# Performance work log

Measured on AMD Instinct MI355X. Metric: run time of the kernel, lower is better.

The kernel has to match this reference:

```python
import jax, jax.numpy as jnp
import numpy as np

# Fixed production-scale dims (equal-size graphs -> no ragged padding needed)
B, NPG, C, H, L, FFN, NC = 16, 512, 128, 8, 4, 512, 4
D = C // H          # head dim = 16
T = NPG + 1         # +1 virtual graph token
EPG = 8192          # edges per graph (avg degree 16)
E = B * EPG


def _ln(x, g, b, eps=1e-5):
    m = x.mean(-1, keepdims=True)
    v = ((x - m) ** 2).mean(-1, keepdims=True)
    return (x - m) * jax.lax.rsqrt(v + eps) * g + b


def setup_inputs() -> dict:
    key = jax.random.key(0)
    ks = jax.random.split(key, 24)
    N = B * NPG
    node_feats = jax.random.normal(ks[0], (N, 3), jnp.float32)
    # intra-graph edges: local endpoints + per-graph node offset (matches batch_ptr math)
    local = jax.random.randint(ks[1], (2, B, EPG), 0, NPG)
    offs = (jnp.arange(B) * NPG)[None, :, None]
    edge_index = (local + offs).reshape(2, E)
    edge_attr = jax.random.randint(ks[2], (E,), 0, 10)

    def nrm(k, shape, scale=0.02):
        return jax.random.normal(k, shape, jnp.float32) * scale

    params = {
        "W_node": nrm(ks[3], (3, C), 0.3), "b_node": jnp.zeros((C,), jnp.float32),
        "graph_token": nrm(ks[4], (C,), 1.0),
        "edge_bias_table": nrm(ks[5], (11, H), 0.1).at[0].set(0.0),  # padding_idx=0
        "in_deg_emb": nrm(ks[6], (512, C)).at[0].set(0.0),           # padding_idx=0
        "out_deg_emb": nrm(ks[7], (512, C)).at[0].set(0.0),
        "vnode_bias": nrm(ks[8], (H,), 1.0),
        "Wq": nrm(ks[9], (L, C, C)), "bq": jnp.zeros((L, C), jnp.float32),
        "Wk": nrm(ks[10], (L, C, C)), "bk": jnp.zeros((L, C), jnp.float32),
        "Wv": nrm(ks[11], (L, C, C)), "bv": jnp.zeros((L, C), jnp.float32),
        "Wo": nrm(ks[12], (L, C, C)), "bo": jnp.zeros((L, C), jnp.float32),
        "ln1_g": jnp.ones((L, C), jnp.float32), "ln1_b": jnp.zeros((L, C), jnp.float32),
        "ln2_g": jnp.ones((L, C), jnp.float32), "ln2_b": jnp.zeros((L, C), jnp.float32),
        "W1": nrm(ks[13], (L, C, FFN)), "b1": jnp.zeros((L, FFN), jnp.float32),
        "W2": nrm(ks[14], (L, FFN, C)), "b2": jnp.zeros((L, C), jnp.float32),
        "normf_g": jnp.ones((C,), jnp.float32), "normf_b": jnp.zeros((C,), jnp.float32),
        "Wc1": nrm(ks[15], (C, C // 2)), "bc1": jnp.zeros((C // 2,), jnp.float32),
        "Wc2": nrm(ks[16], (C // 2, NC)), "bc2": jnp.zeros((NC,), jnp.float32),
    }
    return {"node_feats": node_feats, "edge_index": edge_index,
            "edge_attr": edge_attr, "num_graphs": B, **params}


def reference(node_feats, W_node, b_node, graph_token, edge_bias_table,
              in_deg_emb, out_deg_emb, vnode_bias,
              Wq, bq, Wk, bk, Wv, bv, Wo, bo,
              ln1_g, ln1_b, ln2_g, ln2_b, W1, b1, W2, b2,
              normf_g, normf_b, Wc1, bc1, Wc2, bc2,
              edge_index, edge_attr, num_graphs):
    N = node_feats.shape[0]
    npg = N // num_graphs
    t = npg + 1
    src, dst = edge_index[0], edge_index[1]
    # degree encoders (scatter_add of ones == segment_sum)
    in_deg = jnp.clip(jax.ops.segment_sum(jnp.ones_like(dst), dst, num_segments=N), 0, 511)
    out_deg = jnp.clip(jax.ops.segment_sum(jnp.ones_like(src), src, num_segments=N), 0, 511)
    x_enc = node_feats @ W_node + b_node + in_deg_emb[in_deg] + out_deg_emb[out_deg]
    # equal-size graphs with sorted batch ids -> padding loop is a reshape, mask all-False
    x = jnp.concatenate(
        [jnp.broadcast_to(graph_token, (num_graphs, 1, C)),
         x_enc.reshape(num_graphs, npg, C)], axis=1)  # [B, T, C]
    # attention bias: vnode row/col + scattered edge-attr embeddings
    bias = jnp.zeros((num_graphs, H, t, t), jnp.float32)
    bias = bias.at[:, :, 0, :].set(vnode_bias[None, :, None])
    bias = bias.at[:, :, :, 0].set(vnode_bias[None, :, None])
    eb = edge_bias_table[jnp.clip(edge_attr, 0, 9) + 1]  # [E, H]
    g = src // npg
    sl = src - g * npg + 1
    dl = dst - g * npg + 1
    bias = bias.at[g, :, sl, dl].add(eb)  # duplicate edges accumulate (scatter_add)
    scale = 1.0 / np.sqrt(D).astype(np.float32)
    for l in range(L):  # key_padding_mask is all-False here -> masked_fill is a no-op
        h = _ln(x, ln1_g[l], ln1_b[l])
        q = (h @ Wq[l] + bq[l]).reshape(num_graphs, t, H, D)
        k = (h @ Wk[l] + bk[l]).reshape(num_graphs, t, H, D)
        v = (h @ Wv[l] + bv[l]).reshape(num_graphs, t, H, D)
        scores = jnp.einsum('bthd,bshd->bhts', q, k) * scale + bias
        attn = jax.nn.softmax(scores, axis=-1)
        o = jnp.einsum('bhts,bshd->bthd', attn, v).reshape(num_graphs, t, C)
        x = x + o @ Wo[l] + bo[l]
        h2 = _ln(x, ln2_g[l], ln2_b[l])
        x = x + jax.nn.gelu(h2 @ W1[l] + b1[l], approximate=False) @ W2[l] + b2[l]
    x = _ln(x, normf_g, normf_b)
    gr = x[:, 0, :]  # virtual-node readout
    return jax.nn.gelu(gr @ Wc1 + bc1, approximate=False) @ Wc2 + bc2
```

## Files before the change

### kernel.cpp

```cpp
#include <hip/hip_runtime.h>
#include <hip/hip_bf16.h>

#define BB 16
#define NPG 512
#define CC 128
#define HH 8
#define LL 4
#define FFN 512
#define NCLS 4
#define DD 16
#define TT 513
#define EE 131072
#define NNODES 8192
#define ROWS (BB * TT)
#define ECAP 64
#define SP 544
#define BSTR 292

static constexpr size_t XROWS = (size_t)BB * TT;
static constexpr size_t XSZ   = XROWS * CC;
static constexpr size_t VTSZ  = (size_t)BB * HH * DD * SP;

typedef unsigned short ushort_t;
typedef __attribute__((ext_vector_type(8))) short short8;
typedef __attribute__((ext_vector_type(4))) float floatx4;

__device__ __forceinline__ float gelu_exact(float v) {
    return 0.5f * v * (1.0f + erff(v * 0.70710678118654752440f));
}
__device__ __forceinline__ ushort_t f2bf(float f) {
    union { float f; unsigned u; } c; c.f = f;
    unsigned u = c.u;
    return (ushort_t)((u + 0x7FFFu + ((u >> 16) & 1u)) >> 16);
}
__device__ __forceinline__ int swz(int row, int col, int stride) {
    int kb = col >> 3;
    return row * stride + (((kb ^ (row & 7)) << 3) | (col & 7));
}

__device__ __forceinline__ void qkv_stage4(const ushort_t* hs,
                                           const ushort_t* Wtq, const float* bq_,
                                           const ushort_t* Wtk, const float* bk_,
                                           const ushort_t* Wtv, const float* bv_,
                                           ushort_t* qb, ushort_t* kb, ushort_t* vt,
                                           int m0, int wave, int lq, int quad) {
    const short* hsS = (const short*)hs;
    int n0 = wave * 32;
    int c0 = n0 + lq, c1 = n0 + 16 + lq;
    const short* Ws[3] = {(const short*)Wtq, (const short*)Wtk, (const short*)Wtv};
    const float* bs[3] = {bq_, bk_, bv_};
    size_t rB0 = (size_t)(n0 + lq) * CC, rB1 = (size_t)(n0 + 16 + lq) * CC;

    #pragma unroll
    for (int m = 0; m < 3; ++m) {
        const short* W = Ws[m];
        floatx4 a0 = {0.f,0.f,0.f,0.f}, a1 = a0;
        #pragma unroll
        for (int k0 = 0; k0 < CC; k0 += 32) {
            short8 af = *(const short8*)(hsS + swz(lq, k0 + quad * 8, 128));
            short8 b0 = *(const short8*)(W + rB0 + k0 + quad * 8);
            short8 b1 = *(const short8*)(W + rB1 + k0 + quad * 8);
            a0 = __builtin_amdgcn_mfma_f32_16x16x32_bf16(af, b0, a0, 0, 0, 0);
            a1 = __builtin_amdgcn_mfma_f32_16x16x32_bf16(af, b1, a1, 0, 0, 0);
        }
        float bv0 = bs[m][c0], bv1 = bs[m][c1];
        #pragma unroll
        for (int rg = 0; rg < 4; ++rg) {
            int r = m0 + quad * 4 + rg;
            float v0 = a0[rg] + bv0;
            float v1 = a1[rg] + bv1;
            if (m == 0) {
                qb[(size_t)r * CC + c0] = f2bf(v0 * 0.25f);
                qb[(size_t)r * CC + c1] = f2bf(v1 * 0.25f);
            } else if (m == 1) {
                kb[(size_t)r * CC + c0] = f2bf(v0);
                kb[(size_t)r * CC + c1] = f2bf(v1);
            } else {
                int bg = r / TT;
                int s = r - bg * TT;
                vt[((size_t)(bg * HH + (c0 >> 4)) * DD + (c0 & 15)) * SP + s] = f2bf(v0);
                vt[((size_t)(bg * HH + (c1 >> 4)) * DD + (c1 & 15)) * SP + s] = f2bf(v1);
            }
        }
    }
}

__global__ __launch_bounds__(256) void deg_csr_tr_kernel(const int* __restrict__ ei,
                                                         const int* __restrict__ ea,
                                                         int* __restrict__ deg_in,
                                                         int* __restrict__ deg_out,
                                                         int* __restrict__ cnt,
                                                         int* __restrict__ ebuf,
                                                         const float* __restrict__ Wq,
                                                         const float* __restrict__ Wk,
                                                         const float* __restrict__ Wv,
                                                         const float* __restrict__ Wo,
                                                         const float* __restrict__ W1,
                                                         const float* __restrict__ W2,
                                                         ushort_t* __restrict__ wtqkvo,
                                                         ushort_t* __restrict__ wt1,
                                                         ushort_t* __restrict__ wt2) {
    int bid = blockIdx.x;
    int tid = threadIdx.x;
    if (bid < 512) {
        int e = bid * 256 + tid;
        int src = ei[e], dst = ei[EE + e];
        atomicAdd(&deg_out[src], 1);
        atomicAdd(&deg_in[dst], 1);
        int g = src >> 9;
        int sl = src - (g << 9) + 1;
        int dl = dst - (g << 9) + 1;
        int a = ea[e];
        a = (a < 0) ? 0 : (a > 9 ? 9 : a);
        a += 1;
        int row = g * TT + sl;
        int pos = atomicAdd(&cnt[row], 1);
        if (pos < ECAP) ebuf[(size_t)row * ECAP + pos] = dl | (a << 16);
        return;
    }
    int z = bid - 512;
    const float* src; ushort_t* dst; int K, N, tile;
    if (z < 64) {
        int zz = z >> 2; tile = z & 3;
        int k = zz >> 2, l = zz & 3;
        const float* s4[4] = {Wq, Wk, Wv, Wo};
        src = s4[k] + (size_t)l * CC * CC;
        dst = wtqkvo + (size_t)(k * 4 + l) * 16384;
        K = CC; N = CC;
    } else if (z < 128) {
        int l = (z - 64) >> 4; tile = (z - 64) & 15;
        src = W1 + (size_t)l * CC * FFN;
        dst = wt1 + (size_t)l * 65536;
        K = CC; N = FFN;
    } else {
        int l = (z - 128) >> 4; tile = (z - 128) & 15;
        src = W2 + (size_t)l * FFN * CC;
        dst = wt2 + (size_t)l * 65536;
        K = FFN; N = CC;
    }
    int tilesN = N >> 6;
    int k0 = (tile / tilesN) << 6;
    int n0 = (tile - (tile / tilesN) * tilesN) << 6;
    __shared__ float t[64][65];
    int c = tid & 63, rb = tid >> 6;
    #pragma unroll
    for (int kk = 0; kk < 64; kk += 4)
        t[kk + rb][c] = src[(size_t)(k0 + kk + rb) * N + n0 + c];
    __syncthreads();
    #pragma unroll
    for (int nn = 0; nn < 64; nn += 4)
        dst[(size_t)(n0 + nn + rb) * K + k0 + c] = f2bf(t[c][nn + rb]);
}

__global__ __launch_bounds__(256) void encode_pre_kernel(const float* __restrict__ nf,
                                                         const float* __restrict__ Wn,
                                                         const float* __restrict__ bn,
                                                         const float* __restrict__ gt,
                                                         const float* __restrict__ ide,
                                                         const float* __restrict__ ode,
                                                         const int* __restrict__ deg_in,
                                                         const int* __restrict__ deg_out,
                                                         const float* __restrict__ ln1g_,
                                                         const float* __restrict__ ln1b_,
                                                         const ushort_t* __restrict__ wtqkvo,
                                                         const float* __restrict__ bq_,
                                                         const float* __restrict__ bk_,
                                                         const float* __restrict__ bv_,
                                                         float* __restrict__ x_,
                                                         ushort_t* __restrict__ qb,
                                                         ushort_t* __restrict__ kb,
                                                         ushort_t* __restrict__ vt) {
    int m0 = blockIdx.x * 16;
    int tid = threadIdx.x;
    int wave = tid >> 6, lane = tid & 63, lq = lane & 15, quad = lane >> 4;

    __shared__ ushort_t hs[16 * 128];
    __shared__ float sred[4][16][2];

    int n0 = wave * 32;
    int c0 = n0 + lq, c1 = n0 + 16 + lq;
    float w0[4], w1[4];
    #pragma unroll
    for (int rg = 0; rg < 4; ++rg) {
        int r = m0 + quad * 4 + rg;
        int b = r / TT;
        int t = r - b * TT;
        float v0, v1;
        if (t == 0) {
            v0 = gt[c0]; v1 = gt[c1];
        } else {
            int i = b * NPG + t - 1;
            float f0 = nf[i*3+0], f1 = nf[i*3+1], f2 = nf[i*3+2];
            v0 = bn[c0] + f0*Wn[0*CC + c0] + f1*Wn[1*CC + c0] + f2*Wn[2*CC + c0];
            v1 = bn[c1] + f0*Wn[0*CC + c1] + f1*Wn[1*CC + c1] + f2*Wn[2*CC + c1];
            int di = min(deg_in[i], 511);
            int dq = min(deg_out[i], 511);
            v0 += ide[(size_t)di * CC + c0] + ode[(size_t)dq * CC + c0];
            v1 += ide[(size_t)di * CC + c1] + ode[(size_t)dq * CC + c1];
        }
        x_[(size_t)r * CC + c0] = v0;
        x_[(size_t)r * CC + c1] = v1;
        w0[rg] = v0; w1[rg] = v1;
    }
    #pragma unroll
    for (int rg = 0; rg < 4; ++rg) {
        float s1 = w0[rg] + w1[rg];
        float s2 = w0[rg]*w0[rg] + w1[rg]*w1[rg];
        #pragma unroll
        for (int m = 1; m < 16; m <<= 1) {
            s1 += __shfl_xor(s1, m, 64);
            s2 += __shfl_xor(s2, m, 64);
        }
        if (lq == 0) { sred[wave][quad*4+rg][0] = s1; sred[wave][quad*4+rg][1] = s2; }
    }
    __syncthreads();
    float g0 = ln1g_[c0], g1 = ln1g_[c1], lb0 = ln1b_[c0], lb1 = ln1b_[c1];
    #pragma unroll
    for (int rg = 0; rg < 4; ++rg) {
        int row = quad * 4 + rg;
        float S1 = sred[0][row][0] + sred[1][row][0] + sred[2][row][0] + sred[3][row][0];
        float S2 = sred[0][row][1] + sred[1][row][1] + sred[2][row][1] + sred[3][row][1];
        float mn = S1 * (1.0f/CC);
        float var = S2 * (1.0f/CC) - mn * mn;
        float rs = rsqrtf(var + 1e-5f);
        hs[swz(row, c0, 128)] = f2bf((w0[rg] - mn) * rs * g0 + lb0);
        hs[swz(row, c1, 128)] = f2bf((w1[rg] - mn) * rs * g1 + lb1);
    }
    __syncthreads();
    qkv_stage4(hs, wtqkvo, bq_,
               wtqkvo + (size_t)4 * 16384, bk_,
               wtqkvo + (size_t)8 * 16384, bv_,
               qb, kb, vt, m0, wave, lq, quad);
}

__global__ __launch_bounds__(256) void mega_kernel(const ushort_t* __restrict__ obf,
                                                   const ushort_t* __restrict__ WtO,
                                                   const float* __restrict__ bo_,
                                                   const float* __restrict__ ln2g_,
                                                   const float* __restrict__ ln2b_,
                                                   const ushort_t* __restrict__ Wt1_,
                                                   const float* __restrict__ b1_,
                                                   const ushort_t* __restrict__ Wt2_,
                                                   const float* __restrict__ b2_,
                                                   const float* __restrict__ ln1g_,
                                                   const float* __restrict__ ln1b_,
                                                   const ushort_t* __restrict__ Wtq,
                                                   const float* __restrict__ bq_,
                                                   const ushort_t* __restrict__ Wtk,
                                                   const float* __restrict__ bk_,
                                                   const ushort_t* __restrict__ Wtv,
                                                   const float* __restrict__ bv_,
                                                   const float* __restrict__ nfg,
                                                   const float* __restrict__ nfb,
                                                   const float* __restrict__ Wc1,
                                                   const float* __restrict__ bc1,
                                                   const float* __restrict__ Wc2,
                                                   const float* __restrict__ bc2,
                                                   float* __restrict__ x_,
                                                   ushort_t* __restrict__ qb,
                                                   ushort_t* __restrict__ kb,
                                                   ushort_t* __restrict__ vt,
                                                   float* __restrict__ out,
                                                   int doQKV) {
    int m0 = blockIdx.x * 16;
    int tid = threadIdx.x;
    int wave = tid >> 6, lane = tid & 63, lq = lane & 15, quad = lane >> 4;

    __shared__ ushort_t hs[16 * 128];
    __shared__ ushort_t ms[16 * 512];
    __shared__ float sred[4][16][2];

    int n0 = wave * 32;
    int c0 = n0 + lq, c1 = n0 + 16 + lq;
    float vv0[4], vv1[4];

    {
        const short* Ab = (const short*)obf;
        const short* W = (const short*)WtO;
        size_t rowA = (size_t)(m0 + lq) * CC;
        size_t rB0 = (size_t)(n0 + lq) * CC, rB1 = (size_t)(n0 + 16 + lq) * CC;
        floatx4 a0 = {0.f,0.f,0.f,0.f}, a1 = a0;
        #pragma unroll
        for (int k0 = 0; k0 < CC; k0 += 32) {
            short8 af = *(const short8*)(Ab + rowA + k0 + quad * 8);
            short8 b0 = *(const short8*)(W + rB0 + k0 + quad * 8);
            short8 b1 = *(const short8*)(W + rB1 + k0 + quad * 8);
            a0 = __builtin_amdgcn_mfma_f32_16x16x32_bf16(af, b0, a0, 0, 0, 0);
            a1 = __builtin_amdgcn_mfma_f32_16x16x32_bf16(af, b1, a1, 0, 0, 0);
        }
        float bv0 = bo_[c0], bv1 = bo_[c1];
        #pragma unroll
        for (int rg = 0; rg < 4; ++rg) {
            int r = m0 + quad * 4 + rg;
            vv0[rg] = a0[rg] + bv0 + x_[(size_t)r * CC + c0];
            vv1[rg] = a1[rg] + bv1 + x_[(size_t)r * CC + c1];
        }
        #pragma unroll
        for (int rg = 0; rg < 4; ++rg) {
            float s1 = vv0[rg] + vv1[rg];
            float s2 = vv0[rg]*vv0[rg] + vv1[rg]*vv1[rg];
            #pragma unroll
            for (int m = 1; m < 16; m <<= 1) {
                s1 += __shfl_xor(s1, m, 64);
                s2 += __shfl_xor(s2, m, 64);
            }
            if (lq == 0) { sred[wave][quad*4+rg][0] = s1; sred[wave][quad*4+rg][1] = s2; }
        }
        __syncthreads();
        float g0 = ln2g_[c0], g1 = ln2g_[c1], lb0 = ln2b_[c0], lb1 = ln2b_[c1];
        #pragma unroll
        for (int rg = 0; rg < 4; ++rg) {
            int row = quad * 4 + rg;
            float S1 = sred[0][row][0] + sred[1][row][0] + sred[2][row][0] + sred[3][row][0];
            float S2 = sred[0][row][1] + sred[1][row][1] + sred[2][row][1] + sred[3][row][1];
            float mn = S1 * (1.0f/CC);
            float var = S2 * (1.0f/CC) - mn * mn;
            float rs = rsqrtf(var + 1e-5f);
            hs[swz(row, c0, 128)] = f2bf((vv0[rg] - mn) * rs * g0 + lb0);
            hs[swz(row, c1, 128)] = f2bf((vv1[rg] - mn) * rs * g1 + lb1);
        }
    }
    __syncthreads();

    {
        const short* hsS = (const short*)hs;
        const short* W = (const short*)Wt1_;
        #pragma unroll
        for (int nt = 0; nt < 4; ++nt) {
            int n = wave * 128 + nt * 32;
            size_t rB0 = (size_t)(n + lq) * CC, rB1 = (size_t)(n + 16 + lq) * CC;
            floatx4 a0 = {0.f,0.f,0.f,0.f}, a1 = a0;
            #pragma unroll
            for (int k0 = 0; k0 < CC; k0 += 32) {
                short8 af = *(const short8*)(hsS + swz(lq, k0 + quad * 8, 128));
                short8 b0 = *(const short8*)(W + rB0 + k0 + quad * 8);
                short8 b1 = *(const short8*)(W + rB1 + k0 + quad * 8);
                a0 = __builtin_amdgcn_mfma_f32_16x16x32_bf16(af, b0, a0, 0, 0, 0);
                a1 = __builtin_amdgcn_mfma_f32_16x16x32_bf16(af, b1, a1, 0, 0, 0);
            }
            float bb0 = b1_[n + lq], bb1 = b1_[n + 16 + lq];
            #pragma unroll
            for (int rg = 0; rg < 4; ++rg) {
                int row = quad * 4 + rg;
                ms[swz(row, n + lq, 512)]      = f2bf(gelu_exact(a0[rg] + bb0));
                ms[swz(row, n + 16 + lq, 512)] = f2bf(gelu_exact(a1[rg] + bb1));
            }
        }
    }
    __syncthreads();

    float w0[4], w1[4];
    {
        const short* msS = (const short*)ms;
        const short* W = (const short*)Wt2_;
        size_t rB0 = (size_t)(n0 + lq) * FFN, rB1 = (size_t)(n0 + 16 + lq) * FFN;
        floatx4 a0 = {0.f,0.f,0.f,0.f}, a1 = a0;
        #pragma unroll 8
        for (int k0 = 0; k0 < FFN; k0 += 32) {
            short8 af = *(const short8*)(msS + swz(lq, k0 + quad * 8, 512));
            short8 b0 = *(const short8*)(W + rB0 + k0 + quad * 8);
            short8 b1 = *(const short8*)(W + rB1 + k0 + quad * 8);
            a0 = __builtin_amdgcn_mfma_f32_16x16x32_bf16(af, b0, a0, 0, 0, 0);
            a1 = __builtin_amdgcn_mfma_f32_16x16x32_bf16(af, b1, a1, 0, 0, 0);
        }
        float bv0 = b2_[c0], bv1 = b2_[c1];
        #pragma unroll
        for (int rg = 0; rg < 4; ++rg) {
            int r = m0 + quad * 4 + rg;
            w0[rg] = a0[rg] + bv0 + vv0[rg];
            w1[rg] = a1[rg] + bv1 + vv1[rg];
            x_[(size_t)r * CC + c0] = w0[rg];
            x_[(size_t)r * CC + c1] = w1[rg];
        }
    }

    if (doQKV) {
        #pragma unroll
        for (int rg = 0; rg < 4; ++rg) {
            float s1 = w0[rg] + w1[rg];
            float s2 = w0[rg]*w0[rg] + w1[rg]*w1[rg];
            #pragma unroll
            for (int m = 1; m < 16; m <<= 1) {
                s1 += __shfl_xor(s1, m, 64);
                s2 += __shfl_xor(s2, m, 64);
            }
            if (lq == 0) { sred[wave][quad*4+rg][0] = s1; sred[wave][quad*4+rg][1] = s2; }
        }
        __syncthreads();
        float g0 = ln1g_[c0], g1 = ln1g_[c1], lb0 = ln1b_[c0], lb1 = ln1b_[c1];
        #pragma unroll
        for (int rg = 0; rg < 4; ++rg) {
            int row = quad * 4 + rg;
            float S1 = sred[0][row][0] + sred[1][row][0] + sred[2][row][0] + sred[3][row][0];
            float S2 = sred[0][row][1] + sred[1][row][1] + sred[2][row][1] + sred[3][row][1];
            float mn = S1 * (1.0f/CC);
            float var = S2 * (1.0f/CC) - mn * mn;
            float rs = rsqrtf(var + 1e-5f);
            hs[swz(row, c0, 128)] = f2bf((w0[rg] - mn) * rs * g0 + lb0);
            hs[swz(row, c1, 128)] = f2bf((w1[rg] - mn) * rs * g1 + lb1);
        }
        __syncthreads();
        qkv_stage4(hs, Wtq, bq_, Wtk, bk_, Wtv, bv_, qb, kb, vt, m0, wave, lq, quad);
        return;
    }

    int gb = (m0 + TT - 1) / TT;
    int rgt = gb * TT;
    if (gb >= BB || rgt >= m0 + 16) return;
    int hb = rgt - m0;

    __syncthreads();
    float* hrow = (float*)ms;
    float* xfs  = hrow + CC;
    float* c1s  = xfs + CC;
    float* red  = c1s + 64;
    #pragma unroll
    for (int rg = 0; rg < 4; ++rg) {
        if (quad * 4 + rg == hb) { hrow[c0] = w0[rg]; hrow[c1] = w1[rg]; }
    }
    __syncthreads();

    {
        int c = tid;
        float v = 0.f, s1 = 0.f, s2 = 0.f;
        if (c < CC) { v = hrow[c]; s1 = v; s2 = v * v; }
        #pragma unroll
        for (int m = 32; m >= 1; m >>= 1) {
            s1 += __shfl_xor(s1, m, 64);
            s2 += __shfl_xor(s2, m, 64);
        }
        int w = c >> 6;
        if (c < CC && (c & 63) == 0) { red[w*2] = s1; red[w*2+1] = s2; }
        __syncthreads();
        if (c < CC) {
            float S1 = red[0] + red[2], S2 = red[1] + red[3];
            float mn = S1 * (1.0f/CC);
            float var = S2 * (1.0f/CC) - mn * mn;
            float rs = rsqrtf(var + 1e-5f);
            xfs[c] = (v - mn) * rs * nfg[c] + nfb[c];
        }
        __syncthreads();
        if (c < 64) {
            float acc = bc1[c];
            #pragma unroll 4
            for (int k = 0; k < CC; ++k) acc = fmaf(xfs[k], Wc1[(size_t)k * 64 + c], acc);
            c1s[c] = gelu_exact(acc);
        }
        __syncthreads();
        if (c < NCLS) {
            float acc = bc2[c];
            #pragma unroll 4
            for (int j = 0; j < 64; ++j) acc = fmaf(c1s[j], Wc2[(size_t)j * NCLS + c], acc);
            out[(size_t)gb * NCLS + c] = acc;
        }
    }
}

__global__ __launch_bounds__(256) void attn_kernel(const ushort_t* __restrict__ qb,
                                                   const ushort_t* __restrict__ kb,
                                                   const ushort_t* __restrict__ vt,
                                                   const int* __restrict__ cnt,
                                                   const int* __restrict__ ebuf,
                                                   const float* __restrict__ ebt,
                                                   const float* __restrict__ vnode,
                                                   ushort_t* __restrict__ ob) {
    int bh = blockIdx.x;
    int qt = blockIdx.y;
    int b = bh >> 3, h = bh & (HH - 1);
    int tid = threadIdx.x;
    int wave = tid >> 6, lane = tid & 63, lq = lane & 15, quad = lane >> 4;

    __shared__ float arena[16 * BSTR];
    float* bstrip = arena;

    int qg = qt * 16 + lq;
    int qr = qg < TT ? qg : TT - 1;
    short8 qf = {0,0,0,0,0,0,0,0};
    if (quad < 2)
        qf = *(const short8*)(qb + ((size_t)(b * TT + qr)) * CC + h * DD + quad * 8);
    float vbh = vnode[h];
    int ql = tid >> 4, e0 = tid & 15;
    int qs = qt * 16 + ql;
    int crow = b * TT + (qs < TT ? qs : 0);
    int cn = (qs > 0 && qs < TT) ? min(cnt[crow], ECAP) : 0;

    const short* kbS = (const short*)kb;
    const short* vtS = (const short*)(vt + (size_t)bh * DD * SP);

    floatx4 oacc = {0.f, 0.f, 0.f, 0.f};
    float lsum = 0.f;

    #pragma unroll
    for (int ch = 0; ch < 2; ++ch) {
        int sp_lo = ch ? 9 : 0;
        int sp_hi = ch ? 17 : 9;
        int s_lo  = ch ? 288 : 0;
        int nrows = ch ? 256 : 288;

        int sp = sp_lo + wave;
        short8 af0 = {0,0,0,0,0,0,0,0}, af1 = af0, vf = af0;
        if (sp < sp_hi) {
            int st0 = sp * 2, st1 = sp * 2 + 1;
            int kr0 = min(b * TT + st0 * 16 + lq, (int)XROWS - 1);
            int kr1 = min(b * TT + st1 * 16 + lq, (int)XROWS - 1);
            if (quad < 2) {
                af0 = *(const short8*)(kbS + (size_t)kr0 * CC + h * DD + quad * 8);
                af1 = *(const short8*)(kbS + (size_t)kr1 * CC + h * DD + quad * 8);
            }
            vf = *(const short8*)(vtS + (size_t)lq * SP + sp * 32 + quad * 8);
        }

        for (int i = tid; i < 16 * BSTR / 4; i += 256)
            ((float4*)bstrip)[i] = make_float4(0.f, 0.f, 0.f, 0.f);
        __syncthreads();
        if (ch == 0 && tid < 16) {
            int q = qt * 16 + tid;
            if (q > 0 && q < TT) bstrip[tid * BSTR] = vbh;
        }
        for (int j = e0; j < cn; j += 16) {
            int e = ebuf[(size_t)crow * ECAP + j];
            int dl = e & 0xFFFF, a = e >> 16;
            int loc = dl - s_lo;
            if (loc >= 0 && loc < nrows)
                atomicAdd(&bstrip[ql * BSTR + loc], ebt[a * 8 + h]);
        }
        __syncthreads();

        for (; sp < sp_hi; sp += 4) {
            int spn = sp + 4;
            short8 nf0 = {0,0,0,0,0,0,0,0}, nf1 = nf0, nvf = nf0;
            if (spn < sp_hi) {
                int st0 = spn * 2, st1 = spn * 2 + 1;
                int kr0 = min(b * TT + st0 * 16 + lq, (int)XROWS - 1);
                int kr1 = min(b * TT + st1 * 16 + lq, (int)XROWS - 1);
                if (quad < 2) {
                    nf0 = *(const short8*)(kbS + (size_t)kr0 * CC + h * DD + quad * 8);
                    nf1 = *(const short8*)(kbS + (size_t)kr1 * CC + h * DD + quad * 8);
                }
                nvf = *(const short8*)(vtS + (size_t)lq * SP + spn * 32 + quad * 8);
            }

            unsigned pw[2][2];
            #pragma unroll
            for (int t = 0; t < 2; ++t) {
                int st = sp * 2 + t;
                floatx4 c = __builtin_amdgcn_mfma_f32_16x16x32_bf16(
                    t ? af1 : af0, qf, (floatx4){0.f, 0.f, 0.f, 0.f}, 0, 0, 0);
                float4 bi = *(const float4*)(bstrip + lq * BSTR + (st * 16 - s_lo) + quad * 4);
                float biv[4] = {bi.x, bi.y, bi.z, bi.w};
                float pr[4];
                #pragma unroll
                for (int rg = 0; rg < 4; ++rg) {
                    int s = st * 16 + quad * 4 + rg;
                    float p = 0.f;
                    if (s < TT) p = __expf(c[rg] + biv[rg]);
                    lsum += p;
                    pr[rg] = p;
                }
                pw[t][0] = (unsigned)f2bf(pr[0]) | ((unsigned)f2bf(pr[1]) << 16);
                pw[t][1] = (unsigned)f2bf(pr[2]) | ((unsigned)f2bf(pr[3]) << 16);
            }
            int srcA = lq + (((2 * quad) & 3) << 4);
            int srcB = lq + (((2 * quad + 1) & 3) << 4);
            int a00 = __shfl((int)pw[0][0], srcA, 64);
            int a01 = __shfl((int)pw[0][1], srcA, 64);
            int a10 = __shfl((int)pw[1][0], srcA, 64);
            int a11 = __shfl((int)pw[1][1], srcA, 64);
            int b00 = __shfl((int)pw[0][0], srcB, 64);
            int b01 = __shfl((int)pw[0][1], srcB, 64);
            int b10 = __shfl((int)pw[1][0], srcB, 64);
            int b11 = __shfl((int)pw[1][1], srcB, 64);
            union { int u[4]; short8 s8; } pu;
            bool lo = quad < 2;
            pu.u[0] = lo ? a00 : a10;
            pu.u[1] = lo ? a01 : a11;
            pu.u[2] = lo ? b00 : b10;
            pu.u[3] = lo ? b01 : b11;
            oacc = __builtin_amdgcn_mfma_f32_16x16x32_bf16(vf, pu.s8, oacc, 0, 0, 0);

            af0 = nf0; af1 = nf1; vf = nvf;
        }
        __syncthreads();
    }

    lsum += __shfl_xor(lsum, 16, 64);
    lsum += __shfl_xor(lsum, 32, 64);
    float* redw = arena;
    float* lsumS = arena + 1088;
    #pragma unroll
    for (int rg = 0; rg < 4; ++rg)
        redw[wave * 272 + (quad * 4 + rg) * 17 + lq] = oacc[rg];
    if (quad == 0) lsumS[wave * 16 + lq] = lsum;
    __syncthreads();

    {
        int q = tid >> 4, d = tid & 15;
        float o = 0.f, L = 0.f;
        #pragma unroll
        for (int w = 0; w < 4; ++w) {
            o += redw[w * 272 + d * 17 + q];
            L += lsumS[w * 16 + q];
        }
        int qq = qt * 16 + q;
        if (qq < TT)
            ob[((size_t)(b * TT + qq)) * CC + h * DD + d] = f2bf(o / L);
    }
}

extern "C" void kernel_launch(void* const* d_in, const int* in_sizes, int n_in,
                              void* d_out, int out_size, void* d_ws, size_t ws_size,
                              hipStream_t stream) {
    const float* node_feats = (const float*)d_in[0];
    const int*   edge_index = (const int*)d_in[1];
    const int*   edge_attr  = (const int*)d_in[2];
    const float* W_node  = (const float*)d_in[4];
    const float* b_node  = (const float*)d_in[5];
    const float* g_token = (const float*)d_in[6];
    const float* ebt     = (const float*)d_in[7];
    const float* ide     = (const float*)d_in[8];
    const float* ode     = (const float*)d_in[9];
    const float* vnode   = (const float*)d_in[10];
    const float* Wq = (const float*)d_in[11];
    const float* bq = (const float*)d_in[12];
    const float* Wk = (const float*)d_in[13];
    const float* bk = (const float*)d_in[14];
    const float* Wv = (const float*)d_in[15];
    const float* bv = (const float*)d_in[16];
    const float* Wo = (const float*)d_in[17];
    const float* bo = (const float*)d_in[18];
    const float* ln1g = (const float*)d_in[19];
    const float* ln1b = (const float*)d_in[20];
    const float* ln2g = (const float*)d_in[21];
    const float* ln2b = (const float*)d_in[22];
    const float* W1 = (const float*)d_in[23];
    const float* b1 = (const float*)d_in[24];
    const float* W2 = (const float*)d_in[25];
    const float* b2 = (const float*)d_in[26];
    const float* nfg = (const float*)d_in[27];
    const float* nfb = (const float*)d_in[28];
    const float* Wc1 = (const float*)d_in[29];
    const float* bc1 = (const float*)d_in[30];
    const float* Wc2 = (const float*)d_in[31];
    const float* bc2 = (const float*)d_in[32];
    float* out = (float*)d_out;

    char* base = (char*)d_ws;
    float* x      = (float*)base;     base += XSZ * 4;
    ushort_t* qb  = (ushort_t*)base;  base += XSZ * 2;
    ushort_t* kb  = (ushort_t*)base;  base += XSZ * 2;
    ushort_t* vt  = (ushort_t*)base;  base += VTSZ * 2;
    ushort_t* obf = (ushort_t*)base;  base += XSZ * 2;
    ushort_t* wtqkvo = (ushort_t*)base; base += (size_t)16 * 16384 * 2;
    ushort_t* wt1 = (ushort_t*)base;  base += (size_t)4 * 65536 * 2;
    ushort_t* wt2 = (ushort_t*)base;  base += (size_t)4 * 65536 * 2;
    int* deg_in  = (int*)base;        base += NNODES * 4;
    int* deg_out = (int*)base;        base += NNODES * 4;
    int* cnt     = (int*)base;        base += (size_t)ROWS * 4;
    int* ebuf    = (int*)base;        base += (size_t)ROWS * ECAP * 4;

    const int MT16 = (int)(XROWS / 16);

    hipMemsetAsync(deg_in, 0, (size_t)(2 * NNODES + ROWS) * 4, stream);
    deg_csr_tr_kernel<<<512 + 192, 256, 0, stream>>>(
        edge_index, edge_attr, deg_in, deg_out, cnt, ebuf,
        Wq, Wk, Wv, Wo, W1, W2, wtqkvo, wt1, wt2);

    encode_pre_kernel<<<MT16, 256, 0, stream>>>(
        node_feats, W_node, b_node, g_token, ide, ode, deg_in, deg_out,
        ln1g, ln1b, wtqkvo, bq, bk, bv, x, qb, kb, vt);

    for (int l = 0; l < LL; ++l) {
        attn_kernel<<<dim3(BB*HH, 33), 256, 0, stream>>>(
            qb, kb, vt, cnt, ebuf, ebt, vnode, obf);

        int ln = (l + 1) % LL;
        mega_kernel<<<MT16, 256, 0, stream>>>(
            obf,
            wtqkvo + (size_t)(12 + l)*16384, bo + l*CC,
            ln2g + l*CC, ln2b + l*CC,
            wt1 + (size_t)l*65536, b1 + l*FFN,
            wt2 + (size_t)l*65536, b2 + l*CC,
            ln1g + ln*CC, ln1b + ln*CC,
            wtqkvo + (size_t)(0 + ln)*16384, bq + ln*CC,
            wtqkvo + (size_t)(4 + ln)*16384, bk + ln*CC,
            wtqkvo + (size_t)(8 + ln)*16384, bv + ln*CC,
            nfg, nfb, Wc1, bc1, Wc2, bc2,
            x, qb, kb, vt, out,
            (l < LL-1) ? 1 : 0);
    }
}
```

Baseline: 420.5 us.

## Fuse attention into per-tile layer kernel with double-buffered Q/K/V

Merges the separate attention kernel into the post-attention mega kernel, so each block computes attention for its 16 query rows across all 8 heads. The output stays in shared memory and feeds the Wo projection directly, with no global bf16 round trip. Q/K/V are double-buffered so the next layer's projections can be written while other blocks still read the current ones. Tiles are now per-graph (33×16 grid) and padded rows are skipped. Each block runs the 8 heads one after another, so far fewer blocks are launched (528 versus 4224 attention blocks), which may reduce latency hiding.

```diff
diff --git a/kernel.cpp b/kernel.cpp
--- a/kernel.cpp
+++ b/kernel.cpp
@@ -43,7 +43,7 @@
                                            const ushort_t* Wtk, const float* bk_,
                                            const ushort_t* Wtv, const float* bv_,
                                            ushort_t* qb, ushort_t* kb, ushort_t* vt,
-                                           int m0, int wave, int lq, int quad) {
+                                           int b, int t0, int wave, int lq, int quad) {
     const short* hsS = (const short*)hs;
     int n0 = wave * 32;
     int c0 = n0 + lq, c1 = n0 + 16 + lq;
@@ -66,20 +66,20 @@
         float bv0 = bs[m][c0], bv1 = bs[m][c1];
         #pragma unroll
         for (int rg = 0; rg < 4; ++rg) {
-            int r = m0 + quad * 4 + rg;
+            int t = t0 + quad * 4 + rg;
+            if (t >= TT) continue;
+            size_t r = (size_t)b * TT + t;
             float v0 = a0[rg] + bv0;
             float v1 = a1[rg] + bv1;
             if (m == 0) {
-                qb[(size_t)r * CC + c0] = f2bf(v0 * 0.25f);
-                qb[(size_t)r * CC + c1] = f2bf(v1 * 0.25f);
+                qb[r * CC + c0] = f2bf(v0 * 0.25f);
+                qb[r * CC + c1] = f2bf(v1 * 0.25f);
             } else if (m == 1) {
-                kb[(size_t)r * CC + c0] = f2bf(v0);
-                kb[(size_t)r * CC + c1] = f2bf(v1);
+                kb[r * CC + c0] = f2bf(v0);
+                kb[r * CC + c1] = f2bf(v1);
             } else {
-                int bg = r / TT;
-                int s = r - bg * TT;
-                vt[((size_t)(bg * HH + (c0 >> 4)) * DD + (c0 & 15)) * SP + s] = f2bf(v0);
-                vt[((size_t)(bg * HH + (c1 >> 4)) * DD + (c1 & 15)) * SP + s] = f2bf(v1);
+                vt[((size_t)(b * HH + (c0 >> 4)) * DD + (c0 & 15)) * SP + t] = f2bf(v0);
+                vt[((size_t)(b * HH + (c1 >> 4)) * DD + (c1 & 15)) * SP + t] = f2bf(v1);
             }
         }
     }
@@ -170,7 +170,8 @@
                                                          ushort_t* __restrict__ qb,
                                                          ushort_t* __restrict__ kb,
                                                          ushort_t* __restrict__ vt) {
-    int m0 = blockIdx.x * 16;
+    int qt = blockIdx.x, b = blockIdx.y;
+    int t0 = qt * 16;
     int tid = threadIdx.x;
     int wave = tid >> 6, lane = tid & 63, lq = lane & 15, quad = lane >> 4;
 
@@ -182,14 +183,13 @@
     float w0[4], w1[4];
     #pragma unroll
     for (int rg = 0; rg < 4; ++rg) {
-        int r = m0 + quad * 4 + rg;
-        int b = r / TT;
-        int t = r - b * TT;
+        int t = t0 + quad * 4 + rg;
+        int tc = min(t, TT - 1);
         float v0, v1;
-        if (t == 0) {
+        if (tc == 0) {
             v0 = gt[c0]; v1 = gt[c1];
         } else {
-            int i = b * NPG + t - 1;
+            int i = b * NPG + tc - 1;
             float f0 = nf[i*3+0], f1 = nf[i*3+1], f2 = nf[i*3+2];
             v0 = bn[c0] + f0*Wn[0*CC + c0] + f1*Wn[1*CC + c0] + f2*Wn[2*CC + c0];
             v1 = bn[c1] + f0*Wn[0*CC + c1] + f1*Wn[1*CC + c1] + f2*Wn[2*CC + c1];
@@ -198,8 +198,11 @@
             v0 += ide[(size_t)di * CC + c0] + ode[(size_t)dq * CC + c0];
             v1 += ide[(size_t)di * CC + c1] + ode[(size_t)dq * CC + c1];
         }
-        x_[(size_t)r * CC + c0] = v0;
-        x_[(size_t)r * CC + c1] = v1;
+        if (t < TT) {
+            size_t r = (size_t)b * TT + t;
+            x_[r * CC + c0] = v0;
+            x_[r * CC + c1] = v1;
+        }
         w0[rg] = v0; w1[rg] = v1;
     }
     #pragma unroll
@@ -230,59 +233,212 @@
     qkv_stage4(hs, wtqkvo, bq_,
                wtqkvo + (size_t)4 * 16384, bk_,
                wtqkvo + (size_t)8 * 16384, bv_,
-               qb, kb, vt, m0, wave, lq, quad);
-}
-
-__global__ __launch_bounds__(256) void mega_kernel(const ushort_t* __restrict__ obf,
-                                                   const ushort_t* __restrict__ WtO,
-                                                   const float* __restrict__ bo_,
-                                                   const float* __restrict__ ln2g_,
-                                                   const float* __restrict__ ln2b_,
-                                                   const ushort_t* __restrict__ Wt1_,
-                                                   const float* __restrict__ b1_,
-                                                   const ushort_t* __restrict__ Wt2_,
-                                                   const float* __restrict__ b2_,
-                                                   const float* __restrict__ ln1g_,
-                                                   const float* __restrict__ ln1b_,
-                                                   const ushort_t* __restrict__ Wtq,
-                                                   const float* __restrict__ bq_,
-                                                   const ushort_t* __restrict__ Wtk,
-                                                   const float* __restrict__ bk_,
-                                                   const ushort_t* __restrict__ Wtv,
-                                                   const float* __restrict__ bv_,
-                                                   const float* __restrict__ nfg,
-                                                   const float* __restrict__ nfb,
-                                                   const float* __restrict__ Wc1,
-                                                   const float* __restrict__ bc1,
-                                                   const float* __restrict__ Wc2,
-                                                   const float* __restrict__ bc2,
-                                                   float* __restrict__ x_,
-                                                   ushort_t* __restrict__ qb,
-                                                   ushort_t* __restrict__ kb,
-                                                   ushort_t* __restrict__ vt,
-                                                   float* __restrict__ out,
-                                                   int doQKV) {
-    int m0 = blockIdx.x * 16;
+               qb, kb, vt, b, t0, wave, lq, quad);
+}
+
+__global__ __launch_bounds__(256) void layer_kernel(const ushort_t* __restrict__ qbr,
+                                                    const ushort_t* __restrict__ kbr,
+                                                    const ushort_t* __restrict__ vtr,
+                                                    const int* __restrict__ cnt,
+                                                    const int* __restrict__ ebuf,
+                                                    const float* __restrict__ ebt,
+                                                    const float* __restrict__ vnode,
+                                                    const ushort_t* __restrict__ WtO,
+                                                    const float* __restrict__ bo_,
+                                                    const float* __restrict__ ln2g_,
+                                                    const float* __restrict__ ln2b_,
+                                                    const ushort_t* __restrict__ Wt1_,
+                                                    const float* __restrict__ b1_,
+                                                    const ushort_t* __restrict__ Wt2_,
+                                                    const float* __restrict__ b2_,
+                                                    const float* __restrict__ ln1g_,
+                                                    const float* __restrict__ ln1b_,
+                                                    const ushort_t* __restrict__ Wtq,
+                                                    const float* __restrict__ bq_,
+                                                    const ushort_t* __restrict__ Wtk,
+                                                    const float* __restrict__ bk_,
+                                                    const ushort_t* __restrict__ Wtv,
+                                                    const float* __restrict__ bv_,
+                                                    const float* __restrict__ nfg,
+                                                    const float* __restrict__ nfb,
+                                                    const float* __restrict__ Wc1,
+                                                    const float* __restrict__ bc1,
+                                                    const float* __restrict__ Wc2,
+                                                    const float* __restrict__ bc2,
+                                                    float* __restrict__ x_,
+                                                    ushort_t* __restrict__ qbw,
+                                                    ushort_t* __restrict__ kbw,
+                                                    ushort_t* __restrict__ vtw,
+                                                    float* __restrict__ out,
+                                                    int doQKV) {
+    int qt = blockIdx.x, b = blockIdx.y;
     int tid = threadIdx.x;
     int wave = tid >> 6, lane = tid & 63, lq = lane & 15, quad = lane >> 4;
 
-    __shared__ ushort_t hs[16 * 128];
-    __shared__ ushort_t ms[16 * 512];
+    __shared__ __align__(16) char smem[20480];
+    float* bstrip = (float*)smem;
+    ushort_t* hs = (ushort_t*)smem;
+    ushort_t* ms = (ushort_t*)(smem + 4096);
+    __shared__ __align__(16) ushort_t obs[16 * 128];
     __shared__ float sred[4][16][2];
 
+    int ql = tid >> 4, e0 = tid & 15;
+    int qs = qt * 16 + ql;
+    int crow = b * TT + (qs < TT ? qs : 0);
+    int cn = (qs > 0 && qs < TT) ? min(cnt[crow], ECAP) : 0;
+    int eh[4];
+    #pragma unroll
+    for (int jj = 0; jj < 4; ++jj) {
+        int j = e0 + jj * 16;
+        eh[jj] = (j < cn) ? ebuf[(size_t)crow * ECAP + j] : -1;
+    }
+
+    int qg = qt * 16 + lq;
+    int qr = qg < TT ? qg : TT - 1;
+    const short* kbS = (const short*)kbr;
+
+    for (int h = 0; h < HH; ++h) {
+        __syncthreads();
+        short8 qf = {0,0,0,0,0,0,0,0};
+        if (quad < 2)
+            qf = *(const short8*)(qbr + ((size_t)(b * TT + qr)) * CC + h * DD + quad * 8);
+        float vbh = vnode[h];
+        const short* vtS = (const short*)(vtr + (size_t)(b * HH + h) * DD * SP);
+
+        floatx4 oacc = {0.f, 0.f, 0.f, 0.f};
+        float lsum = 0.f;
+
+        #pragma unroll
+        for (int ch = 0; ch < 2; ++ch) {
+            int sp_lo = ch ? 9 : 0;
+            int sp_hi = ch ? 17 : 9;
+            int s_lo  = ch ? 288 : 0;
+            int nrows = ch ? 256 : 288;
+
+            int sp = sp_lo + wave;
+            short8 af0 = {0,0,0,0,0,0,0,0}, af1 = af0, vf = af0;
+            if (sp < sp_hi) {
+                int st0 = sp * 2, st1 = sp * 2 + 1;
+                int kr0 = min(b * TT + st0 * 16 + lq, (int)XROWS - 1);
+                int kr1 = min(b * TT + st1 * 16 + lq, (int)XROWS - 1);
+                if (quad < 2) {
+                    af0 = *(const short8*)(kbS + (size_t)kr0 * CC + h * DD + quad * 8);
+                    af1 = *(const short8*)(kbS + (size_t)kr1 * CC + h * DD + quad * 8);
+                }
+                vf = *(const short8*)(vtS + (size_t)lq * SP + sp * 32 + quad * 8);
+            }
+
+            for (int i = tid; i < 16 * BSTR / 4; i += 256)
+                ((float4*)bstrip)[i] = make_float4(0.f, 0.f, 0.f, 0.f);
+            __syncthreads();
+            if (ch == 0 && tid < 16) {
+                int q = qt * 16 + tid;
+                if (q > 0 && q < TT) bstrip[tid * BSTR] = vbh;
+            }
+            #pragma unroll
+            for (int jj = 0; jj < 4; ++jj) {
+                int e = eh[jj];
+                if (e >= 0) {
+                    int dl = e & 0xFFFF, a = e >> 16;
+                    int loc = dl - s_lo;
+                    if (loc >= 0 && loc < nrows)
+                        atomicAdd(&bstrip[ql * BSTR + loc], ebt[a * 8 + h]);
+                }
+            }
+            __syncthreads();
+
+            for (; sp < sp_hi; sp += 4) {
+                int spn = sp + 4;
+                short8 nf0 = {0,0,0,0,0,0,0,0}, nf1 = nf0, nvf = nf0;
+                if (spn < sp_hi) {
+                    int st0 = spn * 2, st1 = spn * 2 + 1;
+                    int kr0 = min(b * TT + st0 * 16 + lq, (int)XROWS - 1);
+                    int kr1 = min(b * TT + st1 * 16 + lq, (int)XROWS - 1);
+                    if (quad < 2) {
+                        nf0 = *(const short8*)(kbS + (size_t)kr0 * CC + h * DD + quad * 8);
+                        nf1 = *(const short8*)(kbS + (size_t)kr1 * CC + h * DD + quad * 8);
+                    }
+                    nvf = *(const short8*)(vtS + (size_t)lq * SP + spn * 32 + quad * 8);
+                }
+
+                unsigned pw[2][2];
+                #pragma unroll
+                for (int t = 0; t < 2; ++t) {
+                    int st = sp * 2 + t;
+                    floatx4 c = __builtin_amdgcn_mfma_f32_16x16x32_bf16(
+                        t ? af1 : af0, qf, (floatx4){0.f, 0.f, 0.f, 0.f}, 0, 0, 0);
+                    float4 bi = *(const float4*)(bstrip + lq * BSTR + (st * 16 - s_lo) + quad * 4);
+                    float biv[4] = {bi.x, bi.y, bi.z, bi.w};
+                    float pr[4];
+                    #pragma unroll
+                    for (int rg = 0; rg < 4; ++rg) {
+                        int s = st * 16 + quad * 4 + rg;
+                        float p = 0.f;
+                        if (s < TT) p = __expf(c[rg] + biv[rg]);
+                        lsum += p;
+                        pr[rg] = p;
+                    }
+                    pw[t][0] = (unsigned)f2bf(pr[0]) | ((unsigned)f2bf(pr[1]) << 16);
+                    pw[t][1] = (unsigned)f2bf(pr[2]) | ((unsigned)f2bf(pr[3]) << 16);
+                }
+                int srcA = lq + (((2 * quad) & 3) << 4);
+                int srcB = lq + (((2 * quad + 1) & 3) << 4);
+                int a00 = __shfl((int)pw[0][0], srcA, 64);
+                int a01 = __shfl((int)pw[0][1], srcA, 64);
+                int a10 = __shfl((int)pw[1][0], srcA, 64);
+                int a11 = __shfl((int)pw[1][1], srcA, 64);
+                int b00 = __shfl((int)pw[0][0], srcB, 64);
+                int b01 = __shfl((int)pw[0][1], srcB, 64);
+                int b10 = __shfl((int)pw[1][0], srcB, 64);
+                int b11 = __shfl((int)pw[1][1], srcB, 64);
+                union { int u[4]; short8 s8; } pu;
+                bool lo = quad < 2;
+                pu.u[0] = lo ? a00 : a10;
+                pu.u[1] = lo ? a01 : a11;
+                pu.u[2] = lo ? b00 : b10;
+                pu.u[3] = lo ? b01 : b11;
+                oacc = __builtin_amdgcn_mfma_f32_16x16x32_bf16(vf, pu.s8, oacc, 0, 0, 0);
+
+                af0 = nf0; af1 = nf1; vf = nvf;
+            }
+            __syncthreads();
+        }
+
+        lsum += __shfl_xor(lsum, 16, 64);
+        lsum += __shfl_xor(lsum, 32, 64);
+        float* redw = (float*)smem;
+        float* lsumS = (float*)smem + 1088;
+        #pragma unroll
+        for (int rg = 0; rg < 4; ++rg)
+            redw[wave * 272 + (quad * 4 + rg) * 17 + lq] = oacc[rg];
+        if (quad == 0) lsumS[wave * 16 + lq] = lsum;
+        __syncthreads();
+        {
+            int q = tid >> 4, d = tid & 15;
+            float o = 0.f, L = 0.f;
+            #pragma unroll
+            for (int w = 0; w < 4; ++w) {
+                o += redw[w * 272 + d * 17 + q];
+                L += lsumS[w * 16 + q];
+            }
+            obs[swz(q, h * DD + d, 128)] = f2bf(o / L);
+        }
+    }
+    __syncthreads();
+
+    int t0 = qt * 16;
     int n0 = wave * 32;
     int c0 = n0 + lq, c1 = n0 + 16 + lq;
     float vv0[4], vv1[4];
+    const short* obsS = (const short*)obs;
 
     {
-        const short* Ab = (const short*)obf;
         const short* W = (const short*)WtO;
-        size_t rowA = (size_t)(m0 + lq) * CC;
         size_t rB0 = (size_t)(n0 + lq) * CC, rB1 = (size_t)(n0 + 16 + lq) * CC;
         floatx4 a0 = {0.f,0.f,0.f,0.f}, a1 = a0;
         #pragma unroll
         for (int k0 = 0; k0 < CC; k0 += 32) {
-            short8 af = *(const short8*)(Ab + rowA + k0 + quad * 8);
+            short8 af = *(const short8*)(obsS + swz(lq, k0 + quad * 8, 128));
             short8 b0 = *(const short8*)(W + rB0 + k0 + quad * 8);
             short8 b1 = *(const short8*)(W + rB1 + k0 + quad * 8);
             a0 = __builtin_amdgcn_mfma_f32_16x16x32_bf16(af, b0, a0, 0, 0, 0);
@@ -291,9 +447,10 @@
         float bv0 = bo_[c0], bv1 = bo_[c1];
         #pragma unroll
         for (int rg = 0; rg < 4; ++rg) {
-            int r = m0 + quad * 4 + rg;
-            vv0[rg] = a0[rg] + bv0 + x_[(size_t)r * CC + c0];
-            vv1[rg] = a1[rg] + bv1 + x_[(size_t)r * CC + c1];
+            int t = t0 + quad * 4 + rg;
+            size_t rc = (size_t)b * TT + min(t, TT - 1);
+            vv0[rg] = a0[rg] + bv0 + x_[rc * CC + c0];
+            vv1[rg] = a1[rg] + bv1 + x_[rc * CC + c1];
         }
         #pragma unroll
         for (int rg = 0; rg < 4; ++rg) {
@@ -366,11 +523,14 @@
         float bv0 = b2_[c0], bv1 = b2_[c1];
         #pragma unroll
         for (int rg = 0; rg < 4; ++rg) {
-            int r = m0 + quad * 4 + rg;
+            int t = t0 + quad * 4 + rg;
             w0[rg] = a0[rg] + bv0 + vv0[rg];
             w1[rg] = a1[rg] + bv1 + vv1[rg];
-            x_[(size_t)r * CC + c0] = w0[rg];
-            x_[(size_t)r * CC + c1] = w1[rg];
+            if (t < TT) {
+                size_t r = (size_t)b * TT + t;
+                x_[r * CC + c0] = w0[rg];
+                x_[r * CC + c1] = w1[rg];
+            }
         }
     }
 
@@ -400,14 +560,11 @@
             hs[swz(row, c1, 128)] = f2bf((w1[rg] - mn) * rs * g1 + lb1);
         }
         __syncthreads();
-        qkv_stage4(hs, Wtq, bq_, Wtk, bk_, Wtv, bv_, qb, kb, vt, m0, wave, lq, quad);
+        qkv_stage4(hs, Wtq, bq_, Wtk, bk_, Wtv, bv_, qbw, kbw, vtw, b, t0, wave, lq, quad);
         return;
     }
 
-    int gb = (m0 + TT - 1) / TT;
-    int rgt = gb * TT;
-    if (gb >= BB || rgt >= m0 + 16) return;
-    int hb = rgt - m0;
+    if (qt != 0) return;
 
     __syncthreads();
     float* hrow = (float*)ms;
@@ -416,7 +573,7 @@
     float* red  = c1s + 64;
     #pragma unroll
     for (int rg = 0; rg < 4; ++rg) {
-        if (quad * 4 + rg == hb) { hrow[c0] = w0[rg]; hrow[c1] = w1[rg]; }
+        if (quad * 4 + rg == 0) { hrow[c0] = w0[rg]; hrow[c1] = w1[rg]; }
     }
     __syncthreads();
 
@@ -451,159 +608,8 @@
             float acc = bc2[c];
             #pragma unroll 4
             for (int j = 0; j < 64; ++j) acc = fmaf(c1s[j], Wc2[(size_t)j * NCLS + c], acc);
-            out[(size_t)gb * NCLS + c] = acc;
-        }
-    }
-}
-
-__global__ __launch_bounds__(256) void attn_kernel(const ushort_t* __restrict__ qb,
-                                                   const ushort_t* __restrict__ kb,
-                                                   const ushort_t* __restrict__ vt,
-                                                   const int* __restrict__ cnt,
-                                                   const int* __restrict__ ebuf,
-                                                   const float* __restrict__ ebt,
-                                                   const float* __restrict__ vnode,
-                                                   ushort_t* __restrict__ ob) {
-    int bh = blockIdx.x;
-    int qt = blockIdx.y;
-    int b = bh >> 3, h = bh & (HH - 1);
-    int tid = threadIdx.x;
-    int wave = tid >> 6, lane = tid & 63, lq = lane & 15, quad = lane >> 4;
-
-    __shared__ float arena[16 * BSTR];
-    float* bstrip = arena;
-
-    int qg = qt * 16 + lq;
-    int qr = qg < TT ? qg : TT - 1;
-    short8 qf = {0,0,0,0,0,0,0,0};
-    if (quad < 2)
-        qf = *(const short8*)(qb + ((size_t)(b * TT + qr)) * CC + h * DD + quad * 8);
-    float vbh = vnode[h];
-    int ql = tid >> 4, e0 = tid & 15;
-    int qs = qt * 16 + ql;
-    int crow = b * TT + (qs < TT ? qs : 0);
-    int cn = (qs > 0 && qs < TT) ? min(cnt[crow], ECAP) : 0;
-
-    const short* kbS = (const short*)kb;
-    const short* vtS = (const short*)(vt + (size_t)bh * DD * SP);
-
-    floatx4 oacc = {0.f, 0.f, 0.f, 0.f};
-    float lsum = 0.f;
-
-    #pragma unroll
-    for (int ch = 0; ch < 2; ++ch) {
-        int sp_lo = ch ? 9 : 0;
-        int sp_hi = ch ? 17 : 9;
-        int s_lo  = ch ? 288 : 0;
-        int nrows = ch ? 256 : 288;
-
-        int sp = sp_lo + wave;
-        short8 af0 = {0,0,0,0,0,0,0,0}, af1 = af0, vf = af0;
-        if (sp < sp_hi) {
-            int st0 = sp * 2, st1 = sp * 2 + 1;
-            int kr0 = min(b * TT + st0 * 16 + lq, (int)XROWS - 1);
-            int kr1 = min(b * TT + st1 * 16 + lq, (int)XROWS - 1);
-            if (quad < 2) {
-                af0 = *(const short8*)(kbS + (size_t)kr0 * CC + h * DD + quad * 8);
-                af1 = *(const short8*)(kbS + (size_t)kr1 * CC + h * DD + quad * 8);
-            }
-            vf = *(const short8*)(vtS + (size_t)lq * SP + sp * 32 + quad * 8);
-        }
-
-        for (int i = tid; i < 16 * BSTR / 4; i += 256)
-            ((float4*)bstrip)[i] = make_float4(0.f, 0.f, 0.f, 0.f);
-        __syncthreads();
-        if (ch == 0 && tid < 16) {
-            int q = qt * 16 + tid;
-            if (q > 0 && q < TT) bstrip[tid * BSTR] = vbh;
-        }
-        for (int j = e0; j < cn; j += 16) {
-            int e = ebuf[(size_t)crow * ECAP + j];
-            int dl = e & 0xFFFF, a = e >> 16;
-            int loc = dl - s_lo;
-            if (loc >= 0 && loc < nrows)
-                atomicAdd(&bstrip[ql * BSTR + loc], ebt[a * 8 + h]);
-        }
-        __syncthreads();
-
-        for (; sp < sp_hi; sp += 4) {
-            int spn = sp + 4;
-            short8 nf0 = {0,0,0,0,0,0,0,0}, nf1 = nf0, nvf = nf0;
-            if (spn < sp_hi) {
-                int st0 = spn * 2, st1 = spn * 2 + 1;
-                int kr0 = min(b * TT + st0 * 16 + lq, (int)XROWS - 1);
-                int kr1 = min(b * TT + st1 * 16 + lq, (int)XROWS - 1);
-                if (quad < 2) {
-                    nf0 = *(const short8*)(kbS + (size_t)kr0 * CC + h * DD + quad * 8);
-                    nf1 = *(const short8*)(kbS + (size_t)kr1 * CC + h * DD + quad * 8);
-                }
-                nvf = *(const short8*)(vtS + (size_t)lq * SP + spn * 32 + quad * 8);
-            }
-
-            unsigned pw[2][2];
-            #pragma unroll
-            for (int t = 0; t < 2; ++t) {
-                int st = sp * 2 + t;
-                floatx4 c = __builtin_amdgcn_mfma_f32_16x16x32_bf16(
-                    t ? af1 : af0, qf, (floatx4){0.f, 0.f, 0.f, 0.f}, 0, 0, 0);
-                float4 bi = *(const float4*)(bstrip + lq * BSTR + (st * 16 - s_lo) + quad * 4);
-                float biv[4] = {bi.x, bi.y, bi.z, bi.w};
-                float pr[4];
-                #pragma unroll
-                for (int rg = 0; rg < 4; ++rg) {
-                    int s = st * 16 + quad * 4 + rg;
-                    float p = 0.f;
-                    if (s < TT) p = __expf(c[rg] + biv[rg]);
-                    lsum += p;
-                    pr[rg] = p;
-                }
-                pw[t][0] = (unsigned)f2bf(pr[0]) | ((unsigned)f2bf(pr[1]) << 16);
-                pw[t][1] = (unsigned)f2bf(pr[2]) | ((unsigned)f2bf(pr[3]) << 16);
-            }
-            int srcA = lq + (((2 * quad) & 3) << 4);
-            int srcB = lq + (((2 * quad + 1) & 3) << 4);
-            int a00 = __shfl((int)pw[0][0], srcA, 64);
-            int a01 = __shfl((int)pw[0][1], srcA, 64);
-            int a10 = __shfl((int)pw[1][0], srcA, 64);
-            int a11 = __shfl((int)pw[1][1], srcA, 64);
-            int b00 = __shfl((int)pw[0][0], srcB, 64);
-            int b01 = __shfl((int)pw[0][1], srcB, 64);
-            int b10 = __shfl((int)pw[1][0], srcB, 64);
-            int b11 = __shfl((int)pw[1][1], srcB, 64);
-            union { int u[4]; short8 s8; } pu;
-            bool lo = quad < 2;
-            pu.u[0] = lo ? a00 : a10;
-            pu.u[1] = lo ? a01 : a11;
-            pu.u[2] = lo ? b00 : b10;
-            pu.u[3] = lo ? b01 : b11;
-            oacc = __builtin_amdgcn_mfma_f32_16x16x32_bf16(vf, pu.s8, oacc, 0, 0, 0);
-
-            af0 = nf0; af1 = nf1; vf = nvf;
-        }
-        __syncthreads();
-    }
-
-    lsum += __shfl_xor(lsum, 16, 64);
-    lsum += __shfl_xor(lsum, 32, 64);
-    float* redw = arena;
-    float* lsumS = arena + 1088;
-    #pragma unroll
-    for (int rg = 0; rg < 4; ++rg)
-        redw[wave * 272 + (quad * 4 + rg) * 17 + lq] = oacc[rg];
-    if (quad == 0) lsumS[wave * 16 + lq] = lsum;
-    __syncthreads();
-
-    {
-        int q = tid >> 4, d = tid & 15;
-        float o = 0.f, L = 0.f;
-        #pragma unroll
-        for (int w = 0; w < 4; ++w) {
-            o += redw[w * 272 + d * 17 + q];
-            L += lsumS[w * 16 + q];
-        }
-        int qq = qt * 16 + q;
-        if (qq < TT)
-            ob[((size_t)(b * TT + qq)) * CC + h * DD + d] = f2bf(o / L);
+            out[(size_t)b * NCLS + c] = acc;
+        }
     }
 }
 
@@ -646,10 +652,12 @@
 
     char* base = (char*)d_ws;
     float* x      = (float*)base;     base += XSZ * 4;
-    ushort_t* qb  = (ushort_t*)base;  base += XSZ * 2;
-    ushort_t* kb  = (ushort_t*)base;  base += XSZ * 2;
-    ushort_t* vt  = (ushort_t*)base;  base += VTSZ * 2;
-    ushort_t* obf = (ushort_t*)base;  base += XSZ * 2;
+    ushort_t* qb0 = (ushort_t*)base;  base += XSZ * 2;
+    ushort_t* kb0 = (ushort_t*)base;  base += XSZ * 2;
+    ushort_t* vt0 = (ushort_t*)base;  base += VTSZ * 2;
+    ushort_t* qb1 = (ushort_t*)base;  base += XSZ * 2;
+    ushort_t* kb1 = (ushort_t*)base;  base += XSZ * 2;
+    ushort_t* vt1 = (ushort_t*)base;  base += VTSZ * 2;
     ushort_t* wtqkvo = (ushort_t*)base; base += (size_t)16 * 16384 * 2;
     ushort_t* wt1 = (ushort_t*)base;  base += (size_t)4 * 65536 * 2;
     ushort_t* wt2 = (ushort_t*)base;  base += (size_t)4 * 65536 * 2;
@@ -658,24 +666,24 @@
     int* cnt     = (int*)base;        base += (size_t)ROWS * 4;
     int* ebuf    = (int*)base;        base += (size_t)ROWS * ECAP * 4;
 
-    const int MT16 = (int)(XROWS / 16);
+    ushort_t* qbs[2] = {qb0, qb1};
+    ushort_t* kbs[2] = {kb0, kb1};
+    ushort_t* vts[2] = {vt0, vt1};
 
     hipMemsetAsync(deg_in, 0, (size_t)(2 * NNODES + ROWS) * 4, stream);
     deg_csr_tr_kernel<<<512 + 192, 256, 0, stream>>>(
         edge_index, edge_attr, deg_in, deg_out, cnt, ebuf,
         Wq, Wk, Wv, Wo, W1, W2, wtqkvo, wt1, wt2);
 
-    encode_pre_kernel<<<MT16, 256, 0, stream>>>(
+    encode_pre_kernel<<<dim3(33, BB), 256, 0, stream>>>(
         node_feats, W_node, b_node, g_token, ide, ode, deg_in, deg_out,
-        ln1g, ln1b, wtqkvo, bq, bk, bv, x, qb, kb, vt);
+        ln1g, ln1b, wtqkvo, bq, bk, bv, x, qb0, kb0, vt0);
 
     for (int l = 0; l < LL; ++l) {
-        attn_kernel<<<dim3(BB*HH, 33), 256, 0, stream>>>(
-            qb, kb, vt, cnt, ebuf, ebt, vnode, obf);
-
+        int rd = l & 1, wr = rd ^ 1;
         int ln = (l + 1) % LL;
-        mega_kernel<<<MT16, 256, 0, stream>>>(
-            obf,
+        layer_kernel<<<dim3(33, BB), 256, 0, stream>>>(
+            qbs[rd], kbs[rd], vts[rd], cnt, ebuf, ebt, vnode,
             wtqkvo + (size_t)(12 + l)*16384, bo + l*CC,
             ln2g + l*CC, ln2b + l*CC,
             wt1 + (size_t)l*65536, b1 + l*FFN,
@@ -685,7 +693,7 @@
             wtqkvo + (size_t)(4 + ln)*16384, bk + ln*CC,
             wtqkvo + (size_t)(8 + ln)*16384, bv + ln*CC,
             nfg, nfb, Wc1, bc1, Wc2, bc2,
-            x, qb, kb, vt, out,
+            x, qbs[wr], kbs[wr], vts[wr], out,
             (l < LL-1) ? 1 : 0);
     }
 }
```

Result: slower. 474.2 us (+12.8%).
